# Kernel tuning notes

Hardware: AMD Instinct MI355X
Metric: run time of the kernel (lower is better)

Reference implementation:

```python
import jax, jax.numpy as jnp
import numpy as np

EMBED_DIM = 1024
NUM_HEADS = 16
HEAD_DIM = EMBED_DIM // NUM_HEADS


def setup_inputs() -> dict:
    key = jax.random.key(0)
    ks = jax.random.split(key, 6)
    B, S, D = 2, 2048, EMBED_DIM
    scale = 1.0 / np.sqrt(D)
    return {
        "inputs": jax.random.normal(ks[0], (B, S, D), dtype=jnp.float32),
        "Wq": jax.random.normal(ks[1], (D, D), dtype=jnp.float32) * scale,
        "Wk": jax.random.normal(ks[2], (D, D), dtype=jnp.float32) * scale,
        "Wv": jax.random.normal(ks[3], (D, D), dtype=jnp.float32) * scale,
        "Wo": jax.random.normal(ks[4], (D, D), dtype=jnp.float32) * scale,
        "bo": jnp.zeros((D,), dtype=jnp.float32),
    }


def reference(inputs, Wq, Wk, Wv, Wo, bo):
    B, S, D = inputs.shape
    H, P = NUM_HEADS, HEAD_DIM
    # torch Linear: x @ W.T ; weights stored [out, in]
    q = inputs @ Wq.T
    k = inputs @ Wk.T
    v = inputs @ Wv.T
    # separate heads: [B, S, H, P] -> [B, H, S, P]
    q = q.reshape(B, S, H, P).transpose(0, 2, 1, 3)
    k = k.reshape(B, S, H, P).transpose(0, 2, 1, 3)
    v = v.reshape(B, S, H, P).transpose(0, 2, 1, 3)
    # scaled dot-product attention; scale = 1/sqrt(P + 1e-9)
    scale = 1.0 / jnp.sqrt(jnp.float32(P) + 1e-9)
    scores = jnp.einsum("bhsp,bhtp->bhst", q, k) * scale
    weights = jax.nn.softmax(scores, axis=-1)
    attn = jnp.einsum("bhst,bhtp->bhsp", weights, v)
    # merge heads -> [B, S, D]
    concat = attn.transpose(0, 2, 1, 3).reshape(B, S, D)
    return concat @ Wo.T + bo
```

## Files before the change

### kernel.cpp

```cpp
#include <hip/hip_runtime.h>
#include <hip/hip_bf16.h>

typedef __bf16 bf16;
typedef __bf16 bf16x4 __attribute__((ext_vector_type(4)));
typedef __bf16 bf16x8 __attribute__((ext_vector_type(8)));
typedef short  s16x4  __attribute__((ext_vector_type(4)));
typedef float  f32x4  __attribute__((ext_vector_type(4)));

#define QSCALE 0.18033688011112042f

__device__ __forceinline__ void load16_lds(const bf16* g, bf16* l) {
    __builtin_amdgcn_global_load_lds(
        (const __attribute__((address_space(1))) unsigned int*)g,
        (__attribute__((address_space(3))) unsigned int*)l, 16, 0, 0);
}

__global__ void cvt_f32_bf16(
    const float* __restrict__ s0, const float* __restrict__ s1,
    const float* __restrict__ s2, const float* __restrict__ s3,
    const float* __restrict__ s4,
    bf16* __restrict__ d0, bf16* __restrict__ d1, bf16* __restrict__ d2,
    bf16* __restrict__ d3, bf16* __restrict__ d4)
{
    const float* s; bf16* d; int nblk;
    switch (blockIdx.y) {
        case 0:  s = s0; d = d0; nblk = 2048; break;
        case 1:  s = s1; d = d1; nblk = 512;  break;
        case 2:  s = s2; d = d2; nblk = 512;  break;
        case 3:  s = s3; d = d3; nblk = 512;  break;
        default: s = s4; d = d4; nblk = 512;  break;
    }
    if ((int)blockIdx.x >= nblk) return;
    int idx = blockIdx.x * 256 + threadIdx.x;
    float4 a = ((const float4*)s)[idx * 2];
    float4 b = ((const float4*)s)[idx * 2 + 1];
    bf16x8 o;
    o[0] = (bf16)a.x; o[1] = (bf16)a.y; o[2] = (bf16)a.z; o[3] = (bf16)a.w;
    o[4] = (bf16)b.x; o[5] = (bf16)b.y; o[6] = (bf16)b.z; o[7] = (bf16)b.w;
    *(bf16x8*)&d[idx * 8] = o;
}

__global__ __launch_bounds__(256, 2) void qkv_gemm(
    const bf16* __restrict__ A,
    const bf16* __restrict__ Wq, const bf16* __restrict__ Wk,
    const bf16* __restrict__ Wv,
    bf16* __restrict__ qbuf, bf16* __restrict__ kbuf, bf16* __restrict__ vT)
{
    __shared__ bf16 sA[128 * 32];
    __shared__ bf16 sB[128 * 32];

    const int which = blockIdx.x >> 3;
    const int n0    = (blockIdx.x & 7) * 128;
    const int m0    = blockIdx.y * 128;
    const bf16* B   = (which == 0) ? Wq : (which == 1) ? Wk : Wv;

    const int tid  = threadIdx.x;
    const int lane = tid & 63;
    const int w    = tid >> 6;
    const int wr   = w >> 1, wc = w & 1;
    const int r    = lane & 15;
    const int qd   = lane >> 4;

    f32x4 acc[4][4];
    const f32x4 zero4 = {0.f, 0.f, 0.f, 0.f};
#pragma unroll
    for (int mi = 0; mi < 4; ++mi)
#pragma unroll
        for (int ni = 0; ni < 4; ++ni) acc[mi][ni] = zero4;

    for (int kt = 0; kt < 32; ++kt) {
        const bf16* gA = A + (size_t)m0 * 1024 + kt * 32;
        const bf16* gB = B + (size_t)n0 * 1024 + kt * 32;
        __syncthreads();
#pragma unroll
        for (int j = 0; j < 2; ++j) {
            int task = j * 256 + tid;
            int row  = task >> 2, ch = task & 3;
            int ldsb = (j * 256 + w * 64) * 8;
            load16_lds(gA + (size_t)row * 1024 + ch * 8, &sA[ldsb]);
            load16_lds(gB + (size_t)row * 1024 + ch * 8, &sB[ldsb]);
        }
        __syncthreads();

        bf16x8 af[4], bfr[4];
#pragma unroll
        for (int mi = 0; mi < 4; ++mi)
            af[mi] = *(const bf16x8*)&sA[(wr * 64 + mi * 16 + r) * 32 + qd * 8];
#pragma unroll
        for (int ni = 0; ni < 4; ++ni)
            bfr[ni] = *(const bf16x8*)&sB[(wc * 64 + ni * 16 + r) * 32 + qd * 8];
#pragma unroll
        for (int mi = 0; mi < 4; ++mi)
#pragma unroll
            for (int ni = 0; ni < 4; ++ni)
                acc[mi][ni] = __builtin_amdgcn_mfma_f32_16x16x32_bf16(
                    af[mi], bfr[ni], acc[mi][ni], 0, 0, 0);
    }

    const float scale = (which == 0) ? QSCALE : 1.0f;
#pragma unroll
    for (int mi = 0; mi < 4; ++mi)
#pragma unroll
        for (int ni = 0; ni < 4; ++ni)
#pragma unroll
            for (int i = 0; i < 4; ++i) {
                int row = m0 + wr * 64 + mi * 16 + qd * 4 + i;
                int col = n0 + wc * 64 + ni * 16 + r;
                float v = acc[mi][ni][i] * scale;
                if (which == 0) {
                    qbuf[(size_t)row * 1024 + col] = (bf16)v;
                } else if (which == 1) {
                    kbuf[(size_t)row * 1024 + col] = (bf16)v;
                } else {
                    vT[((size_t)((row >> 11) * 1024 + col)) * 2048 + (row & 2047)] = (bf16)v;
                }
            }
}

__global__ __launch_bounds__(256, 2) void out_gemm(
    const bf16* __restrict__ A, const bf16* __restrict__ B,
    float* __restrict__ C, const float* __restrict__ bias)
{
    __shared__ bf16 sA[128 * 32];
    __shared__ bf16 sB[64 * 32];

    const int tid  = threadIdx.x;
    const int lane = tid & 63;
    const int w    = tid >> 6;
    const int wr   = w >> 1, wc = w & 1;
    const int r    = lane & 15;
    const int qd   = lane >> 4;
    const int m0   = blockIdx.y * 128;
    const int n0   = blockIdx.x * 64;

    f32x4 acc[4][2];
    const f32x4 zero4 = {0.f, 0.f, 0.f, 0.f};
#pragma unroll
    for (int mi = 0; mi < 4; ++mi)
#pragma unroll
        for (int ni = 0; ni < 2; ++ni) acc[mi][ni] = zero4;

    for (int kt = 0; kt < 32; ++kt) {
        const bf16* gA = A + (size_t)m0 * 1024 + kt * 32;
        const bf16* gB = B + (size_t)n0 * 1024 + kt * 32;
        __syncthreads();
#pragma unroll
        for (int j = 0; j < 2; ++j) {
            int task = j * 256 + tid;
            int row  = task >> 2, ch = task & 3;
            int ldsb = (j * 256 + w * 64) * 8;
            load16_lds(gA + (size_t)row * 1024 + ch * 8, &sA[ldsb]);
        }
        {
            int row = tid >> 2, ch = tid & 3;
            int ldsb = (w * 64) * 8;
            load16_lds(gB + (size_t)row * 1024 + ch * 8, &sB[ldsb]);
        }
        __syncthreads();

        bf16x8 af[4], bfr[2];
#pragma unroll
        for (int mi = 0; mi < 4; ++mi)
            af[mi] = *(const bf16x8*)&sA[(wr * 64 + mi * 16 + r) * 32 + qd * 8];
#pragma unroll
        for (int ni = 0; ni < 2; ++ni)
            bfr[ni] = *(const bf16x8*)&sB[(wc * 32 + ni * 16 + r) * 32 + qd * 8];
#pragma unroll
        for (int mi = 0; mi < 4; ++mi)
#pragma unroll
            for (int ni = 0; ni < 2; ++ni)
                acc[mi][ni] = __builtin_amdgcn_mfma_f32_16x16x32_bf16(
                    af[mi], bfr[ni], acc[mi][ni], 0, 0, 0);
    }

#pragma unroll
    for (int mi = 0; mi < 4; ++mi)
#pragma unroll
        for (int ni = 0; ni < 2; ++ni)
#pragma unroll
            for (int i = 0; i < 4; ++i) {
                int row = m0 + wr * 64 + mi * 16 + qd * 4 + i;
                int col = n0 + wc * 32 + ni * 16 + r;
                C[(size_t)row * 1024 + col] = acc[mi][ni][i] + bias[col];
            }
}

__global__ __launch_bounds__(256, 2) void attn_kernel(
    const bf16* __restrict__ qbuf, const bf16* __restrict__ kbuf,
    const bf16* __restrict__ vT, bf16* __restrict__ concat)
{
    __shared__ bf16 sKV[4 * 64 * 72];

    const int tid  = threadIdx.x;
    const int lane = tid & 63;
    const int w    = tid >> 6;
    const int r    = lane & 15;
    const int qd   = lane >> 4;
    const int qt   = blockIdx.x;
    const int bh   = blockIdx.y;
    const int b    = bh >> 4, h = bh & 15;
    const int qrow0 = b * 2048 + qt * 128;
    const size_t vbase = (size_t)bh * 64 * 2048;

    const s16x4 ones4 = {(short)0x3F80, (short)0x3F80, (short)0x3F80, (short)0x3F80};

    int krow[2], kch[2];
#pragma unroll
    for (int t = 0; t < 2; ++t) {
        int flat = t * 256 + tid;
        krow[t] = flat >> 3; kch[t] = flat & 7;
    }

    bf16x8 aq[2][2];
#pragma unroll
    for (int mi = 0; mi < 2; ++mi)
#pragma unroll
        for (int ks = 0; ks < 2; ++ks)
            aq[mi][ks] = *(const bf16x8*)&qbuf[
                (size_t)(qrow0 + w * 32 + mi * 16 + r) * 1024 + h * 64 + ks * 32 + qd * 8];

    f32x4 acc_o[2][4], acc_l[2];
    const f32x4 zero4 = {0.f, 0.f, 0.f, 0.f};
#pragma unroll
    for (int mi = 0; mi < 2; ++mi) {
        acc_l[mi] = zero4;
#pragma unroll
        for (int pj = 0; pj < 4; ++pj) acc_o[mi][pj] = zero4;
    }

    bf16x8 rk[2], rv[2];
#pragma unroll
    for (int t = 0; t < 2; ++t) {
        rk[t] = *(const bf16x8*)&kbuf[(size_t)(b * 2048 + krow[t]) * 1024 + h * 64 + kch[t] * 8];
        rv[t] = *(const bf16x8*)&vT[vbase + (size_t)krow[t] * 2048 + kch[t] * 8];
    }
#pragma unroll
    for (int t = 0; t < 2; ++t) {
        *(bf16x8*)&sKV[0 * 4608 + krow[t] * 72 + kch[t] * 8] = rk[t];
        *(bf16x8*)&sKV[1 * 4608 + krow[t] * 72 + kch[t] * 8] = rv[t];
    }
#pragma unroll
    for (int t = 0; t < 2; ++t) {
        rk[t] = *(const bf16x8*)&kbuf[(size_t)(b * 2048 + 64 + krow[t]) * 1024 + h * 64 + kch[t] * 8];
        rv[t] = *(const bf16x8*)&vT[vbase + (size_t)krow[t] * 2048 + 64 + kch[t] * 8];
    }
    __syncthreads();

    for (int tt = 0; tt < 32; ++tt) {
        {
            int st = (tt + 1) & 1;
#pragma unroll
            for (int t = 0; t < 2; ++t) {
                *(bf16x8*)&sKV[(2 * st + 0) * 4608 + krow[t] * 72 + kch[t] * 8] = rk[t];
                *(bf16x8*)&sKV[(2 * st + 1) * 4608 + krow[t] * 72 + kch[t] * 8] = rv[t];
            }
        }
        {
            int nxt = (tt + 2 < 32) ? tt + 2 : 31;
#pragma unroll
            for (int t = 0; t < 2; ++t) {
                rk[t] = *(const bf16x8*)&kbuf[(size_t)(b * 2048 + nxt * 64 + krow[t]) * 1024 + h * 64 + kch[t] * 8];
                rv[t] = *(const bf16x8*)&vT[vbase + (size_t)krow[t] * 2048 + nxt * 64 + kch[t] * 8];
            }
        }
        const bf16* sK = &sKV[(2 * (tt & 1) + 0) * 4608];
        const bf16* sV = &sKV[(2 * (tt & 1) + 1) * 4608];

        f32x4 accs[2][4];
#pragma unroll
        for (int mi = 0; mi < 2; ++mi)
#pragma unroll
            for (int ni = 0; ni < 4; ++ni) accs[mi][ni] = zero4;
#pragma unroll
        for (int ks = 0; ks < 2; ++ks)
#pragma unroll
            for (int ni = 0; ni < 4; ++ni) {
                bf16x8 ak = *(const bf16x8*)&sK[(ni * 16 + r) * 72 + ks * 32 + qd * 8];
#pragma unroll
                for (int mi = 0; mi < 2; ++mi)
                    accs[mi][ni] = __builtin_amdgcn_mfma_f32_16x16x32_bf16(
                        ak, aq[mi][ks], accs[mi][ni], 0, 0, 0);
            }

        s16x4 pfrag[2][4];
#pragma unroll
        for (int mi = 0; mi < 2; ++mi)
#pragma unroll
            for (int ni = 0; ni < 4; ++ni) {
                bf16x4 pv;
#pragma unroll
                for (int i = 0; i < 4; ++i) pv[i] = (bf16)exp2f(accs[mi][ni][i]);
                pfrag[mi][ni] = __builtin_bit_cast(s16x4, pv);
            }

#pragma unroll
        for (int ni = 0; ni < 4; ++ni) {
#pragma unroll
            for (int pj = 0; pj < 4; ++pj) {
                bf16x4 av = *(const bf16x4*)&sV[(pj * 16 + r) * 72 + ni * 16 + qd * 4];
                s16x4  avs = __builtin_bit_cast(s16x4, av);
#pragma unroll
                for (int mi = 0; mi < 2; ++mi)
                    acc_o[mi][pj] = __builtin_amdgcn_mfma_f32_16x16x16bf16_1k(
                        avs, pfrag[mi][ni], acc_o[mi][pj], 0, 0, 0);
            }
#pragma unroll
            for (int mi = 0; mi < 2; ++mi)
                acc_l[mi] = __builtin_amdgcn_mfma_f32_16x16x16bf16_1k(
                    ones4, pfrag[mi][ni], acc_l[mi], 0, 0, 0);
        }

        __syncthreads();
    }

    bf16* scratch = sKV;
#pragma unroll
    for (int mi = 0; mi < 2; ++mi) {
        float inv = 1.0f / acc_l[mi][0];
        int qloc  = w * 32 + mi * 16 + r;
#pragma unroll
        for (int pj = 0; pj < 4; ++pj)
#pragma unroll
            for (int i = 0; i < 4; ++i)
                scratch[qloc * 72 + pj * 16 + qd * 4 + i] =
                    (bf16)(acc_o[mi][pj][i] * inv);
    }
    __syncthreads();
    {
        int row  = tid >> 1;
        int half = tid & 1;
#pragma unroll
        for (int c = 0; c < 4; ++c) {
            bf16x8 v = *(const bf16x8*)&scratch[row * 72 + half * 32 + c * 8];
            *(bf16x8*)&concat[(size_t)(qrow0 + row) * 1024 + h * 64 + half * 32 + c * 8] = v;
        }
    }
}

extern "C" void kernel_launch(void* const* d_in, const int* in_sizes, int n_in,
                              void* d_out, int out_size, void* d_ws, size_t ws_size,
                              hipStream_t stream)
{
    const float* x  = (const float*)d_in[0];
    const float* Wq = (const float*)d_in[1];
    const float* Wk = (const float*)d_in[2];
    const float* Wv = (const float*)d_in[3];
    const float* Wo = (const float*)d_in[4];
    const float* bo = (const float*)d_in[5];
    float* out = (float*)d_out;

    char* ws = (char*)d_ws;
    bf16* xb     = (bf16*)(ws);
    bf16* Wqb    = (bf16*)(ws + (8u  << 20));
    bf16* Wkb    = (bf16*)(ws + (10u << 20));
    bf16* Wvb    = (bf16*)(ws + (12u << 20));
    bf16* Wob    = (bf16*)(ws + (14u << 20));
    bf16* qbuf   = (bf16*)(ws + (16u << 20));
    bf16* kbuf   = (bf16*)(ws + (24u << 20));
    bf16* vT     = (bf16*)(ws + (32u << 20));
    bf16* concat = (bf16*)(ws + (40u << 20));

    hipLaunchKernelGGL(cvt_f32_bf16, dim3(2048, 5), dim3(256), 0, stream,
                       x, Wq, Wk, Wv, Wo, xb, Wqb, Wkb, Wvb, Wob);
    hipLaunchKernelGGL(qkv_gemm, dim3(24, 32), dim3(256), 0, stream,
                       xb, Wqb, Wkb, Wvb, qbuf, kbuf, vT);
    hipLaunchKernelGGL(attn_kernel, dim3(16, 32), dim3(256), 0, stream,
                       qbuf, kbuf, vT, concat);
    hipLaunchKernelGGL(out_gemm, dim3(16, 32), dim3(256), 0, stream,
                       concat, Wob, out, bo);
}
```

Before: 205.0 us.

## Split attention KV range across two blocks and add a merge kernel

The attention kernel now runs a third grid dimension that splits the 2048 keys into two halves. Each half writes its normalized partial output and its row sums, and a new reduce kernel blends the two halves, weighting each by its share of the row sum. This doubles the number of attention blocks to fill the GPU better, and launch bounds are raised to 4 waves. The QKV GEMM also moves from a K-tile of 32 to 64 to halve its loop iterations and barriers. The split costs an extra kernel launch and extra partial-output traffic, reuses freed workspace (xb and the Wq region), and the higher occupancy target may raise register pressure.

```diff
diff --git a/kernel.cpp b/kernel.cpp
--- a/kernel.cpp
+++ b/kernel.cpp
@@ -46,8 +46,8 @@
     const bf16* __restrict__ Wv,
     bf16* __restrict__ qbuf, bf16* __restrict__ kbuf, bf16* __restrict__ vT)
 {
-    __shared__ bf16 sA[128 * 32];
-    __shared__ bf16 sB[128 * 32];
+    __shared__ bf16 sA[128 * 64];
+    __shared__ bf16 sB[128 * 64];
 
     const int which = blockIdx.x >> 3;
     const int n0    = (blockIdx.x & 7) * 128;
@@ -68,33 +68,36 @@
 #pragma unroll
         for (int ni = 0; ni < 4; ++ni) acc[mi][ni] = zero4;
 
-    for (int kt = 0; kt < 32; ++kt) {
-        const bf16* gA = A + (size_t)m0 * 1024 + kt * 32;
-        const bf16* gB = B + (size_t)n0 * 1024 + kt * 32;
+    for (int kt = 0; kt < 16; ++kt) {
+        const bf16* gA = A + (size_t)m0 * 1024 + kt * 64;
+        const bf16* gB = B + (size_t)n0 * 1024 + kt * 64;
         __syncthreads();
 #pragma unroll
-        for (int j = 0; j < 2; ++j) {
+        for (int j = 0; j < 4; ++j) {
             int task = j * 256 + tid;
-            int row  = task >> 2, ch = task & 3;
+            int row  = task >> 3, ch = task & 7;
             int ldsb = (j * 256 + w * 64) * 8;
             load16_lds(gA + (size_t)row * 1024 + ch * 8, &sA[ldsb]);
             load16_lds(gB + (size_t)row * 1024 + ch * 8, &sB[ldsb]);
         }
         __syncthreads();
 
-        bf16x8 af[4], bfr[4];
-#pragma unroll
-        for (int mi = 0; mi < 4; ++mi)
-            af[mi] = *(const bf16x8*)&sA[(wr * 64 + mi * 16 + r) * 32 + qd * 8];
-#pragma unroll
-        for (int ni = 0; ni < 4; ++ni)
-            bfr[ni] = *(const bf16x8*)&sB[(wc * 64 + ni * 16 + r) * 32 + qd * 8];
-#pragma unroll
-        for (int mi = 0; mi < 4; ++mi)
+#pragma unroll
+        for (int kk = 0; kk < 2; ++kk) {
+            bf16x8 af[4], bfr[4];
+#pragma unroll
+            for (int mi = 0; mi < 4; ++mi)
+                af[mi] = *(const bf16x8*)&sA[(wr * 64 + mi * 16 + r) * 64 + kk * 32 + qd * 8];
 #pragma unroll
             for (int ni = 0; ni < 4; ++ni)
-                acc[mi][ni] = __builtin_amdgcn_mfma_f32_16x16x32_bf16(
-                    af[mi], bfr[ni], acc[mi][ni], 0, 0, 0);
+                bfr[ni] = *(const bf16x8*)&sB[(wc * 64 + ni * 16 + r) * 64 + kk * 32 + qd * 8];
+#pragma unroll
+            for (int mi = 0; mi < 4; ++mi)
+#pragma unroll
+                for (int ni = 0; ni < 4; ++ni)
+                    acc[mi][ni] = __builtin_amdgcn_mfma_f32_16x16x32_bf16(
+                        af[mi], bfr[ni], acc[mi][ni], 0, 0, 0);
+        }
     }
 
     const float scale = (which == 0) ? QSCALE : 1.0f;
@@ -185,9 +188,10 @@
             }
 }
 
-__global__ __launch_bounds__(256, 2) void attn_kernel(
+__global__ __launch_bounds__(256, 4) void attn_kernel(
     const bf16* __restrict__ qbuf, const bf16* __restrict__ kbuf,
-    const bf16* __restrict__ vT, bf16* __restrict__ concat)
+    const bf16* __restrict__ vT,
+    bf16* __restrict__ p0, bf16* __restrict__ p1, float* __restrict__ lbuf)
 {
     __shared__ bf16 sKV[4 * 64 * 72];
 
@@ -198,9 +202,13 @@
     const int qd   = lane >> 4;
     const int qt   = blockIdx.x;
     const int bh   = blockIdx.y;
+    const int z    = blockIdx.z;
     const int b    = bh >> 4, h = bh & 15;
     const int qrow0 = b * 2048 + qt * 128;
+    const int krow0 = b * 2048 + z * 1024;
+    const int vcol0 = z * 1024;
     const size_t vbase = (size_t)bh * 64 * 2048;
+    bf16* pdst = z ? p1 : p0;
 
     const s16x4 ones4 = {(short)0x3F80, (short)0x3F80, (short)0x3F80, (short)0x3F80};
 
@@ -231,8 +239,8 @@
     bf16x8 rk[2], rv[2];
 #pragma unroll
     for (int t = 0; t < 2; ++t) {
-        rk[t] = *(const bf16x8*)&kbuf[(size_t)(b * 2048 + krow[t]) * 1024 + h * 64 + kch[t] * 8];
-        rv[t] = *(const bf16x8*)&vT[vbase + (size_t)krow[t] * 2048 + kch[t] * 8];
+        rk[t] = *(const bf16x8*)&kbuf[(size_t)(krow0 + krow[t]) * 1024 + h * 64 + kch[t] * 8];
+        rv[t] = *(const bf16x8*)&vT[vbase + (size_t)krow[t] * 2048 + vcol0 + kch[t] * 8];
     }
 #pragma unroll
     for (int t = 0; t < 2; ++t) {
@@ -241,12 +249,12 @@
     }
 #pragma unroll
     for (int t = 0; t < 2; ++t) {
-        rk[t] = *(const bf16x8*)&kbuf[(size_t)(b * 2048 + 64 + krow[t]) * 1024 + h * 64 + kch[t] * 8];
-        rv[t] = *(const bf16x8*)&vT[vbase + (size_t)krow[t] * 2048 + 64 + kch[t] * 8];
+        rk[t] = *(const bf16x8*)&kbuf[(size_t)(krow0 + 64 + krow[t]) * 1024 + h * 64 + kch[t] * 8];
+        rv[t] = *(const bf16x8*)&vT[vbase + (size_t)krow[t] * 2048 + vcol0 + 64 + kch[t] * 8];
     }
     __syncthreads();
 
-    for (int tt = 0; tt < 32; ++tt) {
+    for (int tt = 0; tt < 16; ++tt) {
         {
             int st = (tt + 1) & 1;
 #pragma unroll
@@ -256,11 +264,11 @@
             }
         }
         {
-            int nxt = (tt + 2 < 32) ? tt + 2 : 31;
+            int nxt = (tt + 2 < 16) ? tt + 2 : 15;
 #pragma unroll
             for (int t = 0; t < 2; ++t) {
-                rk[t] = *(const bf16x8*)&kbuf[(size_t)(b * 2048 + nxt * 64 + krow[t]) * 1024 + h * 64 + kch[t] * 8];
-                rv[t] = *(const bf16x8*)&vT[vbase + (size_t)krow[t] * 2048 + nxt * 64 + kch[t] * 8];
+                rk[t] = *(const bf16x8*)&kbuf[(size_t)(krow0 + nxt * 64 + krow[t]) * 1024 + h * 64 + kch[t] * 8];
+                rv[t] = *(const bf16x8*)&vT[vbase + (size_t)krow[t] * 2048 + vcol0 + nxt * 64 + kch[t] * 8];
             }
         }
         const bf16* sK = &sKV[(2 * (tt & 1) + 0) * 4608];
@@ -324,6 +332,8 @@
             for (int i = 0; i < 4; ++i)
                 scratch[qloc * 72 + pj * 16 + qd * 4 + i] =
                     (bf16)(acc_o[mi][pj][i] * inv);
+        if (qd == 0)
+            lbuf[(size_t)(z * 4096 + qrow0 + w * 32 + mi * 16 + r) * 16 + h] = acc_l[mi][0];
     }
     __syncthreads();
     {
@@ -332,9 +342,30 @@
 #pragma unroll
         for (int c = 0; c < 4; ++c) {
             bf16x8 v = *(const bf16x8*)&scratch[row * 72 + half * 32 + c * 8];
-            *(bf16x8*)&concat[(size_t)(qrow0 + row) * 1024 + h * 64 + half * 32 + c * 8] = v;
-        }
-    }
+            *(bf16x8*)&pdst[(size_t)(qrow0 + row) * 1024 + h * 64 + half * 32 + c * 8] = v;
+        }
+    }
+}
+
+__global__ void attn_reduce(
+    const bf16* p0, const bf16* p1, const float* __restrict__ lbuf,
+    bf16* concat)
+{
+    int idx = blockIdx.x * 256 + threadIdx.x;
+    int row = idx >> 7;
+    int ch  = idx & 127;
+    int h   = ch >> 3;
+    float l0 = lbuf[(size_t)row * 16 + h];
+    float l1 = lbuf[(size_t)(4096 + row) * 16 + h];
+    float w0 = l0 / (l0 + l1);
+    float w1 = 1.0f - w0;
+    bf16x8 a = *(const bf16x8*)&p0[(size_t)row * 1024 + ch * 8];
+    bf16x8 bb = *(const bf16x8*)&p1[(size_t)row * 1024 + ch * 8];
+    bf16x8 o;
+#pragma unroll
+    for (int i = 0; i < 8; ++i)
+        o[i] = (bf16)(w0 * (float)a[i] + w1 * (float)bb[i]);
+    *(bf16x8*)&concat[(size_t)row * 1024 + ch * 8] = o;
 }
 
 extern "C" void kernel_launch(void* const* d_in, const int* in_sizes, int n_in,
@@ -350,22 +381,26 @@
     float* out = (float*)d_out;
 
     char* ws = (char*)d_ws;
-    bf16* xb     = (bf16*)(ws);
-    bf16* Wqb    = (bf16*)(ws + (8u  << 20));
-    bf16* Wkb    = (bf16*)(ws + (10u << 20));
-    bf16* Wvb    = (bf16*)(ws + (12u << 20));
-    bf16* Wob    = (bf16*)(ws + (14u << 20));
-    bf16* qbuf   = (bf16*)(ws + (16u << 20));
-    bf16* kbuf   = (bf16*)(ws + (24u << 20));
-    bf16* vT     = (bf16*)(ws + (32u << 20));
-    bf16* concat = (bf16*)(ws + (40u << 20));
+    bf16*  xb     = (bf16*)(ws);
+    bf16*  Wqb    = (bf16*)(ws + (8u  << 20));
+    bf16*  Wkb    = (bf16*)(ws + (10u << 20));
+    bf16*  Wvb    = (bf16*)(ws + (12u << 20));
+    bf16*  Wob    = (bf16*)(ws + (14u << 20));
+    bf16*  qbuf   = (bf16*)(ws + (16u << 20));
+    bf16*  kbuf   = (bf16*)(ws + (24u << 20));
+    bf16*  vT     = (bf16*)(ws + (32u << 20));
+    bf16*  concat = (bf16*)(ws + (40u << 20));
+    bf16*  p1     = xb;
+    float* lbuf   = (float*)(ws + (8u << 20));
 
     hipLaunchKernelGGL(cvt_f32_bf16, dim3(2048, 5), dim3(256), 0, stream,
                        x, Wq, Wk, Wv, Wo, xb, Wqb, Wkb, Wvb, Wob);
     hipLaunchKernelGGL(qkv_gemm, dim3(24, 32), dim3(256), 0, stream,
                        xb, Wqb, Wkb, Wvb, qbuf, kbuf, vT);
-    hipLaunchKernelGGL(attn_kernel, dim3(16, 32), dim3(256), 0, stream,
-                       qbuf, kbuf, vT, concat);
+    hipLaunchKernelGGL(attn_kernel, dim3(16, 32, 2), dim3(256), 0, stream,
+                       qbuf, kbuf, vT, concat, p1, lbuf);
+    hipLaunchKernelGGL(attn_reduce, dim3(2048), dim3(256), 0, stream,
+                       concat, p1, lbuf, concat);
     hipLaunchKernelGGL(out_gemm, dim3(16, 32), dim3(256), 0, stream,
                        concat, Wob, out, bo);
 }
```

Result: no change. 205.8 us (+0.4%).
